# Performance work log

Hardware: AMD Instinct MI355X
Metric: run time of the kernel (lower is better)

Reference implementation:

```python
import jax, jax.numpy as jnp
import numpy as np

DIM, HEADS, DEPTH, SEQ, LOCAL_W = 1024, 16, 7, 2048, 64
HEAD_DIM = DIM // HEADS
SCALE = 1.0 / HEAD_DIM ** 0.5


def cantor_mask(S, depth, local_window):
    """Allowed (i,j): |i-j| within local window, OR |i-j| lies in the Cantor set
    under `depth` levels of ternary subdivision (no base-3 digit equals 1)."""
    idx = np.arange(S)
    d = np.abs(idx[:, None] - idx[None, :])
    x = d.copy()
    ok = np.ones_like(d, dtype=bool)
    for _ in range(depth):
        ok &= (x % 3) != 1
        x //= 3
    ok &= x == 0  # offset must be < 3**depth
    return jnp.asarray(ok | (d <= local_window))  # [S, S] bool


def setup_inputs() -> dict:
    key = jax.random.key(0)
    ks = jax.random.split(key, 8)
    B = 2
    s = 0.02
    return {
        "query": jax.random.normal(ks[0], (B, SEQ, DIM), jnp.float32),
        "key_value": jax.random.normal(ks[1], (B, SEQ, DIM), jnp.float32),
        "Wq": jax.random.normal(ks[2], (DIM, DIM), jnp.float32) * s,
        "bq": jnp.zeros((DIM,), jnp.float32),
        "Wkv": jax.random.normal(ks[3], (DIM, 2 * DIM), jnp.float32) * s,
        "bkv": jnp.zeros((2 * DIM,), jnp.float32),
        "Wo": jax.random.normal(ks[4], (DIM, DIM), jnp.float32) * s,
        "bo": jnp.zeros((DIM,), jnp.float32),
    }


def reference(query, key_value, Wq, bq, Wkv, bkv, Wo, bo):
    B, S, D = query.shape
    H, hd = HEADS, HEAD_DIM
    mask = cantor_mask(S, DEPTH, LOCAL_W)  # static [S, S] bool

    q = (query @ Wq + bq).reshape(B, S, H, hd).transpose(0, 2, 1, 3)  # [B,H,S,hd]
    kv = (key_value @ Wkv + bkv).reshape(B, S, 2, H, hd).transpose(2, 0, 3, 1, 4)
    k, v = kv[0], kv[1]  # [B,H,S,hd]

    scores = jnp.einsum("bhqd,bhkd->bhqk", q, k) * SCALE
    scores = jnp.where(mask, scores, jnp.finfo(scores.dtype).min)
    attn = jax.nn.softmax(scores, axis=-1)
    out = jnp.einsum("bhqk,bhkd->bhqd", attn, v)  # [B,H,S,hd]
    out = out.transpose(0, 2, 1, 3).reshape(B, S, D)
    return out @ Wo + bo
```

## Files before the change

### kernel.cpp

```cpp
#include <hip/hip_runtime.h>
#include <stdint.h>

typedef _Float16 half_t;
typedef __attribute__((ext_vector_type(8))) _Float16 half8;
typedef __attribute__((ext_vector_type(4))) _Float16 half4;
typedef __attribute__((ext_vector_type(4))) float floatx4;

#define SEQ 2048
#define NH 16
#define HD 64

#define MFMA16(a, b, c) __builtin_amdgcn_mfma_f32_16x16x16f16(a, b, c, 0, 0, 0)
#define MFMA32K(a, b, c) __builtin_amdgcn_mfma_f32_16x16x32_f16(a, b, c, 0, 0, 0)

#define QSCALE 0.1803368801111306f

__global__ __launch_bounds__(256) void prep(
    const float* __restrict__ query, const float* __restrict__ key_value,
    const float* __restrict__ Wq, const float* __restrict__ Wkv,
    const float* __restrict__ Wo, half_t* __restrict__ xq,
    half_t* __restrict__ xkv, half_t* __restrict__ wqT,
    half_t* __restrict__ wkvT, half_t* __restrict__ woT,
    uint8_t* __restrict__ tok, uint8_t* __restrict__ tok16,
    uint64_t* __restrict__ maskw) {
  int bx = blockIdx.x, tid = threadIdx.x;
  if (bx < 2048) {
    const float* s; half_t* d; int base;
    if (bx < 1024) { s = query; d = xq; base = bx * 4096; }
    else { s = key_value; d = xkv; base = (bx - 1024) * 4096; }
#pragma unroll
    for (int u = 0; u < 4; ++u) {
      int i = base + u * 1024 + tid * 4;
      floatx4 v = *(const floatx4*)(s + i);
      half4 h;
      h[0] = (half_t)v[0]; h[1] = (half_t)v[1];
      h[2] = (half_t)v[2]; h[3] = (half_t)v[3];
      *(half4*)(d + i) = h;
    }
    return;
  }
  if (bx < 4096) {
    __shared__ float tile[32][33];
    int tx = tid & 31, ty = tid >> 5;
    const int K = 1024;
#pragma unroll
    for (int u = 0; u < 2; ++u) {
      int t = (bx - 2048) * 2 + u;
      const float* W; half_t* Wt; int N, nt, kt;
      if (t < 1024) { W = Wq; Wt = wqT; N = 1024; nt = t & 31; kt = t >> 5; }
      else if (t < 3072) { int t2 = t - 1024; W = Wkv; Wt = wkvT; N = 2048; nt = t2 & 63; kt = t2 >> 6; }
      else { int t2 = t - 3072; W = Wo; Wt = woT; N = 1024; nt = t2 & 31; kt = t2 >> 5; }
      int n0 = nt * 32, k0 = kt * 32;
#pragma unroll
      for (int i = 0; i < 4; ++i)
        tile[ty + i * 8][tx] = W[(size_t)(k0 + ty + i * 8) * N + n0 + tx];
      __syncthreads();
#pragma unroll
      for (int i = 0; i < 4; ++i)
        Wt[(size_t)(n0 + ty + i * 8) * K + k0 + tx] = (half_t)tile[tx][ty + i * 8];
      __syncthreads();
    }
    return;
  }
  __shared__ uint8_t slut[2048];
  int ib = bx - 4096;
  for (int d = tid; d < 2048; d += 256) {
    int x = d;
    bool ok = true;
    for (int it = 0; it < 7; ++it) { ok &= ((x % 3) != 1); x /= 3; }
    ok &= (x == 0);
    slut[d] = (ok || d <= 64) ? 1 : 0;
  }
  __syncthreads();
  if (ib == 0) {
    if (tid < 64) {
      int delta = tid - 32;
      int lo = delta * 64 - 63, hi = delta * 64 + 63;
      uint8_t any = 0;
      for (int x = lo; x <= hi; ++x) {
        int a = x < 0 ? -x : x;
        if (a < 2048) any |= slut[a];
      }
      tok[tid] = any;
    }
    {
      int d16 = tid - 128;
      int ctr = d16 * 16;
      uint8_t any = 0;
      for (int x = ctr - 15; x <= ctr + 15; ++x) {
        int a = x < 0 ? -x : x;
        if (a < 2048) any |= slut[a];
      }
      tok16[tid] = any;
    }
  }
  int g = ib * 256 + tid;
  int tt = g - 2048;
  uint64_t w = 0;
  for (int jj = 0; jj < 64; ++jj) {
    int d = tt - jj; d = d < 0 ? -d : d;
    if (d < 2048 && slut[d]) w |= (1ull << jj);
  }
  maskw[g] = w;
}

__device__ __forceinline__ void cp16(half_t* lds, const half_t* g) {
  __builtin_amdgcn_global_load_lds(
      (const __attribute__((address_space(1))) uint32_t*)g,
      (__attribute__((address_space(3))) uint32_t*)lds, 16, 0, 0);
}

__global__ __launch_bounds__(256) void gemm_qkv(
    const half_t* __restrict__ xq, const half_t* __restrict__ xkv,
    const half_t* __restrict__ wqT, const half_t* __restrict__ wkvT,
    const float* __restrict__ bq, const float* __restrict__ bkv,
    half_t* __restrict__ qout, half_t* __restrict__ kout,
    half_t* __restrict__ vTout) {
  extern __shared__ char smemraw[];
  half_t* As = (half_t*)smemraw;
  half_t* Bs = As + 8192;
  const int K = 1024;
  bool isq = blockIdx.y < 8;
  const half_t* A = isq ? xq : xkv;
  const half_t* Bt = isq ? wqT : wkvT;
  const float* bias = isq ? bq : bkv;
  int n0 = (isq ? blockIdx.y : (blockIdx.y - 8)) * 128;
  int m0 = blockIdx.x * 128;

  int tid = threadIdx.x;
  int wave = tid >> 6, lane = tid & 63;
  int c = lane & 15, quad = lane >> 4;
  int wm = (wave >> 1) * 64, wn = (wave & 1) * 64;

  floatx4 acc[4][4] = {};
  int arow = tid >> 2;
  int akc = ((tid & 3) ^ (arow & 3)) * 8;
  int csw = c & 3;

  cp16(&As[wave * 512], A + (size_t)(m0 + arow) * K + akc);
  cp16(&As[2048 + wave * 512], A + (size_t)(m0 + 64 + arow) * K + akc);
  cp16(&Bs[wave * 512], Bt + (size_t)(n0 + arow) * K + akc);
  cp16(&Bs[2048 + wave * 512], Bt + (size_t)(n0 + 64 + arow) * K + akc);

  for (int kt = 0; kt < 32; ++kt) {
    __syncthreads();
    if (kt + 1 < 32) {
      int k0 = (kt + 1) * 32;
      int b = (kt + 1) & 1;
      cp16(&As[b * 4096 + wave * 512], A + (size_t)(m0 + arow) * K + k0 + akc);
      cp16(&As[b * 4096 + 2048 + wave * 512], A + (size_t)(m0 + 64 + arow) * K + k0 + akc);
      cp16(&Bs[b * 4096 + wave * 512], Bt + (size_t)(n0 + arow) * K + k0 + akc);
      cp16(&Bs[b * 4096 + 2048 + wave * 512], Bt + (size_t)(n0 + 64 + arow) * K + k0 + akc);
    }
    int b = kt & 1;
    half8 af[4], bf[4];
#pragma unroll
    for (int mt = 0; mt < 4; ++mt)
      af[mt] = *(const half8*)&As[b * 4096 + (wm + mt * 16 + c) * 32 + ((quad ^ csw) * 8)];
#pragma unroll
    for (int nt = 0; nt < 4; ++nt)
      bf[nt] = *(const half8*)&Bs[b * 4096 + (wn + nt * 16 + c) * 32 + ((quad ^ csw) * 8)];
#pragma unroll
    for (int mt = 0; mt < 4; ++mt)
#pragma unroll
      for (int nt = 0; nt < 4; ++nt)
        acc[mt][nt] = MFMA32K(af[mt], bf[nt], acc[mt][nt]);
  }

  __syncthreads();
  half_t* ep = (half_t*)smemraw;
  int bb = m0 >> 11, sbase = m0 & 2047;
  bool isv = (!isq) && (n0 >= 1024);

  if (!isv) {
#pragma unroll
    for (int nt = 0; nt < 4; ++nt) {
      int nl = wn + nt * 16 + c;
      float bv = bias[n0 + nl];
#pragma unroll
      for (int mt = 0; mt < 4; ++mt)
#pragma unroll
        for (int r = 0; r < 4; ++r) {
          int ml = wm + mt * 16 + quad * 4 + r;
          float v = acc[mt][nt][r] + bv;
          if (isq) v *= QSCALE;
          ep[ml * 128 + nl] = (half_t)v;
        }
    }
    __syncthreads();
    half_t* outp = isq ? qout : kout;
#pragma unroll
    for (int rd = 0; rd < 8; ++rd) {
      int id = rd * 256 + tid;
      int ml = id >> 4, ch = id & 15;
      int ng = n0 + ch * 8;
      int h = ng >> 6, d0 = ng & 63;
      half8 v = *(const half8*)&ep[ml * 128 + ch * 8];
      *(half8*)(outp + ((size_t)(bb * 16 + h) * SEQ + sbase + ml) * 64 + d0) = v;
    }
  } else {
#pragma unroll
    for (int nt = 0; nt < 4; ++nt) {
      int nl = wn + nt * 16 + c;
      float bv = bias[n0 + nl];
#pragma unroll
      for (int mt = 0; mt < 4; ++mt) {
        int ml = wm + mt * 16 + quad * 4;
        half4 hv;
#pragma unroll
        for (int r = 0; r < 4; ++r) hv[r] = (half_t)(acc[mt][nt][r] + bv);
        *(half4*)&ep[nl * 136 + ml] = hv;
      }
    }
    __syncthreads();
#pragma unroll
    for (int rd = 0; rd < 8; ++rd) {
      int id = rd * 256 + tid;
      int nl = id >> 4, mc = id & 15;
      int ng = n0 + nl;
      int h = (ng >> 6) & 15, d = ng & 63;
      half8 v = *(const half8*)&ep[nl * 136 + mc * 8];
      *(half8*)(vTout + ((size_t)(bb * 16 + h) * 64 + d) * SEQ + sbase + mc * 8) = v;
    }
  }
}

__global__ __launch_bounds__(256) void gemm_out(
    const half_t* __restrict__ A, const half_t* __restrict__ Bt,
    const float* __restrict__ bias, float* __restrict__ outf) {
  __shared__ half_t As[2][128 * 32];
  __shared__ half_t Bs[2][64 * 32];
  const int K = 1024;
  int tid = threadIdx.x;
  int wave = tid >> 6, lane = tid & 63;
  int c = lane & 15, quad = lane >> 4;
  int wm = (wave >> 1) * 64, wn = (wave & 1) * 32;
  int m0 = blockIdx.x * 128, n0 = blockIdx.y * 64;

  floatx4 acc[4][2] = {};
  int arow = tid >> 2;
  int akc = ((tid & 3) ^ (arow & 3)) * 8;
  int csw = c & 3;

  cp16(&As[0][wave * 512], A + (size_t)(m0 + arow) * K + akc);
  cp16(&As[0][2048 + wave * 512], A + (size_t)(m0 + 64 + arow) * K + akc);
  cp16(&Bs[0][wave * 512], Bt + (size_t)(n0 + arow) * K + akc);

  for (int kt = 0; kt < 32; ++kt) {
    __syncthreads();
    if (kt + 1 < 32) {
      int k0 = (kt + 1) * 32;
      int b = (kt + 1) & 1;
      cp16(&As[b][wave * 512], A + (size_t)(m0 + arow) * K + k0 + akc);
      cp16(&As[b][2048 + wave * 512], A + (size_t)(m0 + 64 + arow) * K + k0 + akc);
      cp16(&Bs[b][wave * 512], Bt + (size_t)(n0 + arow) * K + k0 + akc);
    }
    int b = kt & 1;
    half8 af[4], bf[2];
#pragma unroll
    for (int mt = 0; mt < 4; ++mt)
      af[mt] = *(const half8*)&As[b][(wm + mt * 16 + c) * 32 + ((quad ^ csw) * 8)];
#pragma unroll
    for (int nt = 0; nt < 2; ++nt)
      bf[nt] = *(const half8*)&Bs[b][(wn + nt * 16 + c) * 32 + ((quad ^ csw) * 8)];
#pragma unroll
    for (int mt = 0; mt < 4; ++mt)
#pragma unroll
      for (int nt = 0; nt < 2; ++nt)
        acc[mt][nt] = MFMA32K(af[mt], bf[nt], acc[mt][nt]);
  }

#pragma unroll
  for (int nt = 0; nt < 2; ++nt) {
    int n = n0 + wn + nt * 16 + c;
    float bv = bias[n];
#pragma unroll
    for (int mt = 0; mt < 4; ++mt)
#pragma unroll
      for (int r = 0; r < 4; ++r) {
        int m = m0 + wm + mt * 16 + quad * 4 + r;
        outf[(size_t)m * 1024 + n] = acc[mt][nt][r] + bv;
      }
  }
}

__global__ __launch_bounds__(512) void attn_kernel(
    const half_t* __restrict__ qb, const half_t* __restrict__ kb,
    const half_t* __restrict__ vTg, half_t* __restrict__ ctx,
    const uint64_t* __restrict__ maskw, const uint8_t* __restrict__ tok,
    const uint8_t* __restrict__ tok16g) {
  __shared__ half_t kT[64 * 64];
  __shared__ half_t vT[64 * 64];
  __shared__ half_t ot[128 * 72];
  __shared__ int list[34];
  __shared__ uint8_t tok16s[256];

  int tid = threadIdx.x, wave = tid >> 6, lane = tid & 63;
  int c = lane & 15, q = lane >> 4;
  int id = blockIdx.x;
  int bh = (id & 7) * 4 + ((id >> 3) & 3);
  int it128 = id >> 5;
  int i0 = it128 << 7;
  const half_t* qbase = qb + (size_t)bh * SEQ * HD;
  const half_t* kg = kb + (size_t)bh * SEQ * HD;
  const half_t* vg = vTg + (size_t)bh * HD * SEQ;

  if (tid < 256) tok16s[tid] = tok16g[tid];
  if (wave == 0) {
    int jt = lane;
    int base = i0 >> 6;
    bool act = (jt < 32) &&
               (tok[(jt - base) + 32] | tok[(jt - base - 1) + 32]);
    unsigned long long bal = __ballot(act);
    if (act) {
      int pre = __popcll(bal & ((1ull << jt) - 1));
      list[1 + pre] = jt << 6;
    }
    if (lane == 0) list[0] = __popcll(bal);
  }

  int i_row = i0 + wave * 16 + c;
  int it16 = (i0 >> 4) + wave;
  half8 qf0 = *(const half8*)(qbase + (size_t)i_row * 64 + q * 8);
  half8 qf1 = *(const half8*)(qbase + (size_t)i_row * 64 + 32 + q * 8);

  floatx4 oacc[4] = {};
  floatx4 lacc = {};
  half4 ones;
  ones[0] = (half_t)1.f; ones[1] = (half_t)1.f;
  ones[2] = (half_t)1.f; ones[3] = (half_t)1.f;

  int srow = tid >> 3;
  int sch = tid & 7;
  int ssw = srow & 7;

  __syncthreads();
  int nact = list[0];
  int j0 = list[1];

  half8 kr = *(const half8*)(kg + (size_t)(j0 + srow) * 64 + sch * 8);
  half8 vr = *(const half8*)(vg + (size_t)srow * SEQ + j0 + sch * 8);
  uint64_t wcur = maskw[(i_row - j0) + 2048];

  for (int ti = 0; ti < nact; ++ti) {
    int bidx = (j0 >> 4) - it16 + 128;
    __syncthreads();
    *(half8*)&kT[srow * 64 + ((sch ^ ssw) * 8)] = kr;
    *(half8*)&vT[srow * 64 + ((sch ^ ssw) * 8)] = vr;
    int j0n = (ti + 1 < nact) ? list[2 + ti] : j0;
    __syncthreads();

    uint64_t wnext = wcur;
    if (ti + 1 < nact) {
      kr = *(const half8*)(kg + (size_t)(j0n + srow) * 64 + sch * 8);
      vr = *(const half8*)(vg + (size_t)srow * SEQ + j0n + sch * 8);
      wnext = maskw[(i_row - j0n) + 2048];
    }

    uint32_t wlo = (uint32_t)(wcur >> (4 * q));
    uint32_t whi = (uint32_t)(wcur >> (32 + 4 * q));
#pragma unroll
    for (int jt = 0; jt < 4; ++jt) {
      if (!tok16s[bidx + jt]) continue;
      int row = jt * 16 + c;
      int sw = c & 7;
      half8 a0 = *(const half8*)&kT[row * 64 + ((q ^ sw) * 8)];
      half8 a1 = *(const half8*)&kT[row * 64 + (((4 + q) ^ sw) * 8)];
      floatx4 t = {};
      t = MFMA32K(a0, qf0, t);
      t = MFMA32K(a1, qf1, t);
      uint32_t ww = (jt < 2) ? wlo : whi;
#pragma unroll
      for (int r = 0; r < 4; ++r) {
        float p = __builtin_exp2f(t[r]);
        int bitpos = 16 * (jt & 1) + r;
        uint32_t msk = (uint32_t)(((int)(ww << (31 - bitpos))) >> 31);
        t[r] = __uint_as_float(__float_as_uint(p) & msk);
      }
      auto lo = __builtin_amdgcn_cvt_pkrtz(t[0], t[1]);
      auto hi = __builtin_amdgcn_cvt_pkrtz(t[2], t[3]);
      half4 pb;
      pb[0] = lo[0]; pb[1] = lo[1]; pb[2] = hi[0]; pb[3] = hi[1];
      lacc = MFMA16(ones, pb, lacc);
#pragma unroll
      for (int mt = 0; mt < 4; ++mt) {
        int drow = mt * 16 + c;
        int ch = 2 * jt + (q >> 1);
        half4 a = *(const half4*)&vT[drow * 64 + ((ch ^ sw) * 8) + (q & 1) * 4];
        oacc[mt] = MFMA16(a, pb, oacc[mt]);
      }
    }
    wcur = wnext;
    j0 = j0n;
  }

  float inv_l = 1.0f / lacc[0];
#pragma unroll
  for (int mt = 0; mt < 4; ++mt)
#pragma unroll
    for (int r = 0; r < 4; ++r)
      ot[(wave * 16 + c) * 72 + mt * 16 + 4 * q + r] = (half_t)(oacc[mt][r] * inv_l);
  __syncthreads();
  {
    int row = tid >> 2, chq = tid & 3;
    int b = bh >> 4, h = bh & 15;
    size_t base = (((size_t)(b * SEQ + i0 + row) * NH) + h) * 64 + chq * 16;
    half8 v0 = *(const half8*)&ot[row * 72 + chq * 16];
    half8 v1 = *(const half8*)&ot[row * 72 + chq * 16 + 8];
    *(half8*)(ctx + base) = v0;
    *(half8*)(ctx + base + 8) = v1;
  }
}

extern "C" void kernel_launch(void* const* d_in, const int* in_sizes, int n_in,
                              void* d_out, int out_size, void* d_ws, size_t ws_size,
                              hipStream_t stream) {
  const float* query = (const float*)d_in[0];
  const float* key_value = (const float*)d_in[1];
  const float* Wq = (const float*)d_in[2];
  const float* bq = (const float*)d_in[3];
  const float* Wkv = (const float*)d_in[4];
  const float* bkv = (const float*)d_in[5];
  const float* Wo = (const float*)d_in[6];
  const float* bo = (const float*)d_in[7];

  char* ws = (char*)d_ws;
  uint8_t* tok = (uint8_t*)ws;
  uint8_t* tok16 = (uint8_t*)(ws + 1024);
  uint64_t* maskw = (uint64_t*)(ws + 4096);
  const size_t MB = 1ull << 20;
  half_t* xq = (half_t*)(ws + 1 * MB);
  half_t* xkv = (half_t*)(ws + 9 * MB);
  half_t* wqT = (half_t*)(ws + 17 * MB);
  half_t* wkvT = (half_t*)(ws + 19 * MB);
  half_t* woT = (half_t*)(ws + 23 * MB);
  half_t* qbuf = (half_t*)(ws + 25 * MB);
  half_t* kbuf = (half_t*)(ws + 33 * MB);
  half_t* vTg = (half_t*)(ws + 41 * MB);
  half_t* ctx = xq;

  hipLaunchKernelGGL(prep, dim3(4112), dim3(256), 0, stream,
                     query, key_value, Wq, Wkv, Wo, xq, xkv, wqT, wkvT, woT,
                     tok, tok16, maskw);
  hipLaunchKernelGGL(gemm_qkv, dim3(32, 24), dim3(256), 34816, stream,
                     xq, xkv, wqT, wkvT, bq, bkv, qbuf, kbuf, vTg);
  hipLaunchKernelGGL(attn_kernel, dim3(512), dim3(512), 0, stream,
                     qbuf, kbuf, vTg, ctx, maskw, tok, tok16);
  hipLaunchKernelGGL(gemm_out, dim3(32, 16), dim3(256), 0, stream,
                     ctx, woT, bo, (float*)d_out);
}
```

Baseline: 215.5 us.

## Fuse QKV GEMM, attention and output GEMM into one persistent kernel with grid barriers

Replaces the three kernel launches after prep with one persistent kernel of 512 blocks of 512 threads. Blocks pull GEMM tiles from an atomic work counter and pass through software grid barriers between phases. The QKV GEMM tile grows to 128x256 and the output GEMM tile to 128x128. The aim is to remove launch gaps and tail effects between stages, at the cost of spin-wait barriers and a co-residency requirement that risks deadlock if all 512 blocks cannot be resident at once.

```diff
diff --git a/kernel.cpp b/kernel.cpp
--- a/kernel.cpp
+++ b/kernel.cpp
@@ -22,7 +22,7 @@
     half_t* __restrict__ xkv, half_t* __restrict__ wqT,
     half_t* __restrict__ wkvT, half_t* __restrict__ woT,
     uint8_t* __restrict__ tok, uint8_t* __restrict__ tok16,
-    uint64_t* __restrict__ maskw) {
+    uint64_t* __restrict__ maskw, uint32_t* __restrict__ ctrs) {
   int bx = blockIdx.x, tid = threadIdx.x;
   if (bx < 2048) {
     const float* s; half_t* d; int base;
@@ -64,6 +64,7 @@
   }
   __shared__ uint8_t slut[2048];
   int ib = bx - 4096;
+  if (ib == 0 && tid < 8) ctrs[tid] = 0;
   for (int d = tid; d < 2048; d += 256) {
     int x = d;
     bool ok = true;
@@ -110,305 +111,335 @@
       (__attribute__((address_space(3))) uint32_t*)lds, 16, 0, 0);
 }
 
-__global__ __launch_bounds__(256) void gemm_qkv(
+__device__ __forceinline__ void gridbar(uint32_t* ctr, uint32_t target) {
+  __threadfence();
+  __syncthreads();
+  if (threadIdx.x == 0) {
+    atomicAdd(ctr, 1u);
+    while (atomicAdd(ctr, 0u) < target) __builtin_amdgcn_s_sleep(16);
+  }
+  __syncthreads();
+  __threadfence();
+}
+
+__global__ __launch_bounds__(512, 4) void fused(
     const half_t* __restrict__ xq, const half_t* __restrict__ xkv,
     const half_t* __restrict__ wqT, const half_t* __restrict__ wkvT,
     const float* __restrict__ bq, const float* __restrict__ bkv,
     half_t* __restrict__ qout, half_t* __restrict__ kout,
-    half_t* __restrict__ vTout) {
+    half_t* __restrict__ vTout, const uint64_t* __restrict__ maskw,
+    const uint8_t* __restrict__ tok, const uint8_t* __restrict__ tok16g,
+    half_t* __restrict__ ctx, const half_t* __restrict__ woT,
+    const float* __restrict__ bo, float* __restrict__ outf,
+    uint32_t* ctrs) {
   extern __shared__ char smemraw[];
-  half_t* As = (half_t*)smemraw;
-  half_t* Bs = As + 8192;
-  const int K = 1024;
-  bool isq = blockIdx.y < 8;
-  const half_t* A = isq ? xq : xkv;
-  const half_t* Bt = isq ? wqT : wkvT;
-  const float* bias = isq ? bq : bkv;
-  int n0 = (isq ? blockIdx.y : (blockIdx.y - 8)) * 128;
-  int m0 = blockIdx.x * 128;
+  __shared__ int s_t;
+  __shared__ int list[34];
+  __shared__ uint8_t tok16s[256];
 
   int tid = threadIdx.x;
   int wave = tid >> 6, lane = tid & 63;
   int c = lane & 15, quad = lane >> 4;
-  int wm = (wave >> 1) * 64, wn = (wave & 1) * 64;
-
-  floatx4 acc[4][4] = {};
-  int arow = tid >> 2;
-  int akc = ((tid & 3) ^ (arow & 3)) * 8;
-  int csw = c & 3;
-
-  cp16(&As[wave * 512], A + (size_t)(m0 + arow) * K + akc);
-  cp16(&As[2048 + wave * 512], A + (size_t)(m0 + 64 + arow) * K + akc);
-  cp16(&Bs[wave * 512], Bt + (size_t)(n0 + arow) * K + akc);
-  cp16(&Bs[2048 + wave * 512], Bt + (size_t)(n0 + 64 + arow) * K + akc);
-
-  for (int kt = 0; kt < 32; ++kt) {
+  const int K = 1024;
+
+  {
+    half_t* As = (half_t*)smemraw;
+    half_t* Bs = As + 8192;
+    int wm = (wave >> 2) * 64, wn = (wave & 3) * 64;
+    int arow = tid >> 2;
+    int akc = ((tid & 3) ^ (arow & 3)) * 8;
+    int csw = c & 3;
+    for (;;) {
+      if (tid == 0) s_t = (int)atomicAdd(&ctrs[1], 1u);
+      __syncthreads();
+      int t = s_t;
+      __syncthreads();
+      if (t >= 384) break;
+      int xt = t & 31, y = t >> 5;
+      bool isq = y < 4;
+      const half_t* A = isq ? xq : xkv;
+      const half_t* Bt = isq ? wqT : wkvT;
+      const float* bias = isq ? bq : bkv;
+      int n0 = isq ? y * 256 : (y - 4) * 256;
+      int m0 = xt * 128;
+
+      floatx4 acc[4][4] = {};
+      cp16(&As[tid * 8], A + (size_t)(m0 + arow) * K + akc);
+      cp16(&Bs[tid * 8], Bt + (size_t)(n0 + arow) * K + akc);
+      cp16(&Bs[4096 + tid * 8], Bt + (size_t)(n0 + 128 + arow) * K + akc);
+
+      for (int kt = 0; kt < 32; ++kt) {
+        __syncthreads();
+        if (kt + 1 < 32) {
+          int k0 = (kt + 1) * 32;
+          int b = (kt + 1) & 1;
+          cp16(&As[b * 4096 + tid * 8], A + (size_t)(m0 + arow) * K + k0 + akc);
+          cp16(&Bs[b * 8192 + tid * 8], Bt + (size_t)(n0 + arow) * K + k0 + akc);
+          cp16(&Bs[b * 8192 + 4096 + tid * 8], Bt + (size_t)(n0 + 128 + arow) * K + k0 + akc);
+        }
+        int b = kt & 1;
+        half8 af[4], bf[4];
+#pragma unroll
+        for (int mt = 0; mt < 4; ++mt)
+          af[mt] = *(const half8*)&As[b * 4096 + (wm + mt * 16 + c) * 32 + ((quad ^ csw) * 8)];
+#pragma unroll
+        for (int nt = 0; nt < 4; ++nt)
+          bf[nt] = *(const half8*)&Bs[b * 8192 + (wn + nt * 16 + c) * 32 + ((quad ^ csw) * 8)];
+#pragma unroll
+        for (int mt = 0; mt < 4; ++mt)
+#pragma unroll
+          for (int nt = 0; nt < 4; ++nt)
+            acc[mt][nt] = MFMA32K(af[mt], bf[nt], acc[mt][nt]);
+      }
+
+      __syncthreads();
+      half_t* ep = (half_t*)smemraw;
+      int bb = m0 >> 11, sbase = m0 & 2047;
+      bool isv = (!isq) && (n0 >= 1024);
+#pragma unroll
+      for (int nh = 0; nh < 2; ++nh) {
+        if (!isv) {
+          if ((wn >> 7) == nh) {
+            int wnl = wn & 127;
+#pragma unroll
+            for (int nt = 0; nt < 4; ++nt) {
+              int nl = wnl + nt * 16 + c;
+              float bv = bias[n0 + wn + nt * 16 + c];
+#pragma unroll
+              for (int mt = 0; mt < 4; ++mt)
+#pragma unroll
+                for (int r = 0; r < 4; ++r) {
+                  int ml = wm + mt * 16 + quad * 4 + r;
+                  float v = acc[mt][nt][r] + bv;
+                  if (isq) v *= QSCALE;
+                  ep[ml * 128 + nl] = (half_t)v;
+                }
+            }
+          }
+          __syncthreads();
+          half_t* outp = isq ? qout : kout;
+#pragma unroll
+          for (int rd = 0; rd < 4; ++rd) {
+            int id = rd * 512 + tid;
+            int ml = id >> 4, ch = id & 15;
+            int ng = n0 + nh * 128 + ch * 8;
+            int h = ng >> 6, d0 = ng & 63;
+            half8 v = *(const half8*)&ep[ml * 128 + ch * 8];
+            *(half8*)(outp + ((size_t)(bb * 16 + h) * SEQ + sbase + ml) * 64 + d0) = v;
+          }
+          __syncthreads();
+        } else {
+          if ((wn >> 7) == nh) {
+            int wnl = wn & 127;
+#pragma unroll
+            for (int nt = 0; nt < 4; ++nt) {
+              int nl = wnl + nt * 16 + c;
+              float bv = bias[n0 + wn + nt * 16 + c];
+#pragma unroll
+              for (int mt = 0; mt < 4; ++mt) {
+                int ml = wm + mt * 16 + quad * 4;
+                half4 hv;
+#pragma unroll
+                for (int r = 0; r < 4; ++r) hv[r] = (half_t)(acc[mt][nt][r] + bv);
+                *(half4*)&ep[nl * 136 + ml] = hv;
+              }
+            }
+          }
+          __syncthreads();
+#pragma unroll
+          for (int rd = 0; rd < 4; ++rd) {
+            int id = rd * 512 + tid;
+            int nl = id >> 4, mc = id & 15;
+            int ng = n0 + nh * 128 + nl;
+            int h = (ng >> 6) & 15, d = ng & 63;
+            half8 v = *(const half8*)&ep[nl * 136 + mc * 8];
+            *(half8*)(vTout + ((size_t)(bb * 16 + h) * 64 + d) * SEQ + sbase + mc * 8) = v;
+          }
+          __syncthreads();
+        }
+      }
+    }
+  }
+
+  gridbar(&ctrs[0], 512);
+
+  {
+    half_t* kT = (half_t*)smemraw;
+    half_t* vT = kT + 4096;
+    half_t* ot = vT + 4096;
+    int id = blockIdx.x;
+    int bh = (id & 7) * 4 + ((id >> 3) & 3);
+    int it128 = id >> 5;
+    int i0 = it128 << 7;
+    const half_t* qbase = qout + (size_t)bh * SEQ * HD;
+    const half_t* kg = kout + (size_t)bh * SEQ * HD;
+    const half_t* vg = vTout + (size_t)bh * HD * SEQ;
+
+    if (tid < 256) tok16s[tid] = tok16g[tid];
+    if (wave == 0) {
+      int jt = lane;
+      int base = i0 >> 6;
+      bool act = (jt < 32) &&
+                 (tok[(jt - base) + 32] | tok[(jt - base - 1) + 32]);
+      unsigned long long bal = __ballot(act);
+      if (act) {
+        int pre = __popcll(bal & ((1ull << jt) - 1));
+        list[1 + pre] = jt << 6;
+      }
+      if (lane == 0) list[0] = __popcll(bal);
+    }
+
+    int i_row = i0 + wave * 16 + c;
+    int it16 = (i0 >> 4) + wave;
+    half8 qf0 = *(const half8*)(qbase + (size_t)i_row * 64 + quad * 8);
+    half8 qf1 = *(const half8*)(qbase + (size_t)i_row * 64 + 32 + quad * 8);
+
+    floatx4 oacc[4] = {};
+    floatx4 lacc = {};
+    half4 ones;
+    ones[0] = (half_t)1.f; ones[1] = (half_t)1.f;
+    ones[2] = (half_t)1.f; ones[3] = (half_t)1.f;
+
+    int srow = tid >> 3;
+    int sch = tid & 7;
+    int ssw = srow & 7;
+
     __syncthreads();
-    if (kt + 1 < 32) {
-      int k0 = (kt + 1) * 32;
-      int b = (kt + 1) & 1;
-      cp16(&As[b * 4096 + wave * 512], A + (size_t)(m0 + arow) * K + k0 + akc);
-      cp16(&As[b * 4096 + 2048 + wave * 512], A + (size_t)(m0 + 64 + arow) * K + k0 + akc);
-      cp16(&Bs[b * 4096 + wave * 512], Bt + (size_t)(n0 + arow) * K + k0 + akc);
-      cp16(&Bs[b * 4096 + 2048 + wave * 512], Bt + (size_t)(n0 + 64 + arow) * K + k0 + akc);
-    }
-    int b = kt & 1;
-    half8 af[4], bf[4];
+    int nact = list[0];
+    int j0 = list[1];
+
+    half8 kr = *(const half8*)(kg + (size_t)(j0 + srow) * 64 + sch * 8);
+    half8 vr = *(const half8*)(vg + (size_t)srow * SEQ + j0 + sch * 8);
+    uint64_t wcur = maskw[(i_row - j0) + 2048];
+
+    for (int ti = 0; ti < nact; ++ti) {
+      int bidx = (j0 >> 4) - it16 + 128;
+      __syncthreads();
+      *(half8*)&kT[srow * 64 + ((sch ^ ssw) * 8)] = kr;
+      *(half8*)&vT[srow * 64 + ((sch ^ ssw) * 8)] = vr;
+      int j0n = (ti + 1 < nact) ? list[2 + ti] : j0;
+      __syncthreads();
+
+      uint64_t wnext = wcur;
+      if (ti + 1 < nact) {
+        kr = *(const half8*)(kg + (size_t)(j0n + srow) * 64 + sch * 8);
+        vr = *(const half8*)(vg + (size_t)srow * SEQ + j0n + sch * 8);
+        wnext = maskw[(i_row - j0n) + 2048];
+      }
+
+      uint32_t wlo = (uint32_t)(wcur >> (4 * quad));
+      uint32_t whi = (uint32_t)(wcur >> (32 + 4 * quad));
+#pragma unroll
+      for (int jt = 0; jt < 4; ++jt) {
+        if (!tok16s[bidx + jt]) continue;
+        int row = jt * 16 + c;
+        int sw = c & 7;
+        half8 a0 = *(const half8*)&kT[row * 64 + ((quad ^ sw) * 8)];
+        half8 a1 = *(const half8*)&kT[row * 64 + (((4 + quad) ^ sw) * 8)];
+        floatx4 tt = {};
+        tt = MFMA32K(a0, qf0, tt);
+        tt = MFMA32K(a1, qf1, tt);
+        uint32_t ww = (jt < 2) ? wlo : whi;
+#pragma unroll
+        for (int r = 0; r < 4; ++r) {
+          float p = __builtin_exp2f(tt[r]);
+          int bitpos = 16 * (jt & 1) + r;
+          uint32_t msk = (uint32_t)(((int)(ww << (31 - bitpos))) >> 31);
+          tt[r] = __uint_as_float(__float_as_uint(p) & msk);
+        }
+        auto lo = __builtin_amdgcn_cvt_pkrtz(tt[0], tt[1]);
+        auto hi = __builtin_amdgcn_cvt_pkrtz(tt[2], tt[3]);
+        half4 pb;
+        pb[0] = lo[0]; pb[1] = lo[1]; pb[2] = hi[0]; pb[3] = hi[1];
+        lacc = MFMA16(ones, pb, lacc);
+#pragma unroll
+        for (int mt = 0; mt < 4; ++mt) {
+          int drow = mt * 16 + c;
+          int ch = 2 * jt + (quad >> 1);
+          half4 a = *(const half4*)&vT[drow * 64 + ((ch ^ sw) * 8) + (quad & 1) * 4];
+          oacc[mt] = MFMA16(a, pb, oacc[mt]);
+        }
+      }
+      wcur = wnext;
+      j0 = j0n;
+    }
+
+    float inv_l = 1.0f / lacc[0];
 #pragma unroll
     for (int mt = 0; mt < 4; ++mt)
-      af[mt] = *(const half8*)&As[b * 4096 + (wm + mt * 16 + c) * 32 + ((quad ^ csw) * 8)];
-#pragma unroll
-    for (int nt = 0; nt < 4; ++nt)
-      bf[nt] = *(const half8*)&Bs[b * 4096 + (wn + nt * 16 + c) * 32 + ((quad ^ csw) * 8)];
-#pragma unroll
-    for (int mt = 0; mt < 4; ++mt)
-#pragma unroll
-      for (int nt = 0; nt < 4; ++nt)
-        acc[mt][nt] = MFMA32K(af[mt], bf[nt], acc[mt][nt]);
-  }
-
-  __syncthreads();
-  half_t* ep = (half_t*)smemraw;
-  int bb = m0 >> 11, sbase = m0 & 2047;
-  bool isv = (!isq) && (n0 >= 1024);
-
-  if (!isv) {
-#pragma unroll
-    for (int nt = 0; nt < 4; ++nt) {
-      int nl = wn + nt * 16 + c;
-      float bv = bias[n0 + nl];
-#pragma unroll
-      for (int mt = 0; mt < 4; ++mt)
-#pragma unroll
-        for (int r = 0; r < 4; ++r) {
-          int ml = wm + mt * 16 + quad * 4 + r;
-          float v = acc[mt][nt][r] + bv;
-          if (isq) v *= QSCALE;
-          ep[ml * 128 + nl] = (half_t)v;
+#pragma unroll
+      for (int r = 0; r < 4; ++r)
+        ot[(wave * 16 + c) * 72 + mt * 16 + 4 * quad + r] = (half_t)(oacc[mt][r] * inv_l);
+    __syncthreads();
+    {
+      int row = tid >> 2, chq = tid & 3;
+      int b = bh >> 4, h = bh & 15;
+      size_t base = (((size_t)(b * SEQ + i0 + row) * NH) + h) * 64 + chq * 16;
+      half8 v0 = *(const half8*)&ot[row * 72 + chq * 16];
+      half8 v1 = *(const half8*)&ot[row * 72 + chq * 16 + 8];
+      *(half8*)(ctx + base) = v0;
+      *(half8*)(ctx + base + 8) = v1;
+    }
+  }
+
+  gridbar(&ctrs[0], 1024);
+
+  {
+    half_t* As = (half_t*)smemraw;
+    half_t* Bs = As + 8192;
+    int wm = (wave >> 2) * 64, wn = (wave & 3) * 32;
+    int arow = tid >> 2;
+    int akc = ((tid & 3) ^ (arow & 3)) * 8;
+    int csw = c & 3;
+    for (;;) {
+      if (tid == 0) s_t = (int)atomicAdd(&ctrs[2], 1u);
+      __syncthreads();
+      int t = s_t;
+      __syncthreads();
+      if (t >= 256) break;
+      int m0 = (t & 31) * 128, n0 = (t >> 5) * 128;
+
+      floatx4 acc[4][2] = {};
+      cp16(&As[tid * 8], ctx + (size_t)(m0 + arow) * K + akc);
+      cp16(&Bs[tid * 8], woT + (size_t)(n0 + arow) * K + akc);
+
+      for (int kt = 0; kt < 32; ++kt) {
+        __syncthreads();
+        if (kt + 1 < 32) {
+          int k0 = (kt + 1) * 32;
+          int b = (kt + 1) & 1;
+          cp16(&As[b * 4096 + tid * 8], ctx + (size_t)(m0 + arow) * K + k0 + akc);
+          cp16(&Bs[b * 4096 + tid * 8], woT + (size_t)(n0 + arow) * K + k0 + akc);
         }
-    }
-    __syncthreads();
-    half_t* outp = isq ? qout : kout;
-#pragma unroll
-    for (int rd = 0; rd < 8; ++rd) {
-      int id = rd * 256 + tid;
-      int ml = id >> 4, ch = id & 15;
-      int ng = n0 + ch * 8;
-      int h = ng >> 6, d0 = ng & 63;
-      half8 v = *(const half8*)&ep[ml * 128 + ch * 8];
-      *(half8*)(outp + ((size_t)(bb * 16 + h) * SEQ + sbase + ml) * 64 + d0) = v;
-    }
-  } else {
-#pragma unroll
-    for (int nt = 0; nt < 4; ++nt) {
-      int nl = wn + nt * 16 + c;
-      float bv = bias[n0 + nl];
-#pragma unroll
-      for (int mt = 0; mt < 4; ++mt) {
-        int ml = wm + mt * 16 + quad * 4;
-        half4 hv;
-#pragma unroll
-        for (int r = 0; r < 4; ++r) hv[r] = (half_t)(acc[mt][nt][r] + bv);
-        *(half4*)&ep[nl * 136 + ml] = hv;
-      }
-    }
-    __syncthreads();
-#pragma unroll
-    for (int rd = 0; rd < 8; ++rd) {
-      int id = rd * 256 + tid;
-      int nl = id >> 4, mc = id & 15;
-      int ng = n0 + nl;
-      int h = (ng >> 6) & 15, d = ng & 63;
-      half8 v = *(const half8*)&ep[nl * 136 + mc * 8];
-      *(half8*)(vTout + ((size_t)(bb * 16 + h) * 64 + d) * SEQ + sbase + mc * 8) = v;
-    }
-  }
-}
-
-__global__ __launch_bounds__(256) void gemm_out(
-    const half_t* __restrict__ A, const half_t* __restrict__ Bt,
-    const float* __restrict__ bias, float* __restrict__ outf) {
-  __shared__ half_t As[2][128 * 32];
-  __shared__ half_t Bs[2][64 * 32];
-  const int K = 1024;
-  int tid = threadIdx.x;
-  int wave = tid >> 6, lane = tid & 63;
-  int c = lane & 15, quad = lane >> 4;
-  int wm = (wave >> 1) * 64, wn = (wave & 1) * 32;
-  int m0 = blockIdx.x * 128, n0 = blockIdx.y * 64;
-
-  floatx4 acc[4][2] = {};
-  int arow = tid >> 2;
-  int akc = ((tid & 3) ^ (arow & 3)) * 8;
-  int csw = c & 3;
-
-  cp16(&As[0][wave * 512], A + (size_t)(m0 + arow) * K + akc);
-  cp16(&As[0][2048 + wave * 512], A + (size_t)(m0 + 64 + arow) * K + akc);
-  cp16(&Bs[0][wave * 512], Bt + (size_t)(n0 + arow) * K + akc);
-
-  for (int kt = 0; kt < 32; ++kt) {
-    __syncthreads();
-    if (kt + 1 < 32) {
-      int k0 = (kt + 1) * 32;
-      int b = (kt + 1) & 1;
-      cp16(&As[b][wave * 512], A + (size_t)(m0 + arow) * K + k0 + akc);
-      cp16(&As[b][2048 + wave * 512], A + (size_t)(m0 + 64 + arow) * K + k0 + akc);
-      cp16(&Bs[b][wave * 512], Bt + (size_t)(n0 + arow) * K + k0 + akc);
-    }
-    int b = kt & 1;
-    half8 af[4], bf[2];
-#pragma unroll
-    for (int mt = 0; mt < 4; ++mt)
-      af[mt] = *(const half8*)&As[b][(wm + mt * 16 + c) * 32 + ((quad ^ csw) * 8)];
-#pragma unroll
-    for (int nt = 0; nt < 2; ++nt)
-      bf[nt] = *(const half8*)&Bs[b][(wn + nt * 16 + c) * 32 + ((quad ^ csw) * 8)];
-#pragma unroll
-    for (int mt = 0; mt < 4; ++mt)
-#pragma unroll
-      for (int nt = 0; nt < 2; ++nt)
-        acc[mt][nt] = MFMA32K(af[mt], bf[nt], acc[mt][nt]);
-  }
-
-#pragma unroll
-  for (int nt = 0; nt < 2; ++nt) {
-    int n = n0 + wn + nt * 16 + c;
-    float bv = bias[n];
-#pragma unroll
-    for (int mt = 0; mt < 4; ++mt)
-#pragma unroll
-      for (int r = 0; r < 4; ++r) {
-        int m = m0 + wm + mt * 16 + quad * 4 + r;
-        outf[(size_t)m * 1024 + n] = acc[mt][nt][r] + bv;
-      }
-  }
-}
-
-__global__ __launch_bounds__(512) void attn_kernel(
-    const half_t* __restrict__ qb, const half_t* __restrict__ kb,
-    const half_t* __restrict__ vTg, half_t* __restrict__ ctx,
-    const uint64_t* __restrict__ maskw, const uint8_t* __restrict__ tok,
-    const uint8_t* __restrict__ tok16g) {
-  __shared__ half_t kT[64 * 64];
-  __shared__ half_t vT[64 * 64];
-  __shared__ half_t ot[128 * 72];
-  __shared__ int list[34];
-  __shared__ uint8_t tok16s[256];
-
-  int tid = threadIdx.x, wave = tid >> 6, lane = tid & 63;
-  int c = lane & 15, q = lane >> 4;
-  int id = blockIdx.x;
-  int bh = (id & 7) * 4 + ((id >> 3) & 3);
-  int it128 = id >> 5;
-  int i0 = it128 << 7;
-  const half_t* qbase = qb + (size_t)bh * SEQ * HD;
-  const half_t* kg = kb + (size_t)bh * SEQ * HD;
-  const half_t* vg = vTg + (size_t)bh * HD * SEQ;
-
-  if (tid < 256) tok16s[tid] = tok16g[tid];
-  if (wave == 0) {
-    int jt = lane;
-    int base = i0 >> 6;
-    bool act = (jt < 32) &&
-               (tok[(jt - base) + 32] | tok[(jt - base - 1) + 32]);
-    unsigned long long bal = __ballot(act);
-    if (act) {
-      int pre = __popcll(bal & ((1ull << jt) - 1));
-      list[1 + pre] = jt << 6;
-    }
-    if (lane == 0) list[0] = __popcll(bal);
-  }
-
-  int i_row = i0 + wave * 16 + c;
-  int it16 = (i0 >> 4) + wave;
-  half8 qf0 = *(const half8*)(qbase + (size_t)i_row * 64 + q * 8);
-  half8 qf1 = *(const half8*)(qbase + (size_t)i_row * 64 + 32 + q * 8);
-
-  floatx4 oacc[4] = {};
-  floatx4 lacc = {};
-  half4 ones;
-  ones[0] = (half_t)1.f; ones[1] = (half_t)1.f;
-  ones[2] = (half_t)1.f; ones[3] = (half_t)1.f;
-
-  int srow = tid >> 3;
-  int sch = tid & 7;
-  int ssw = srow & 7;
-
-  __syncthreads();
-  int nact = list[0];
-  int j0 = list[1];
-
-  half8 kr = *(const half8*)(kg + (size_t)(j0 + srow) * 64 + sch * 8);
-  half8 vr = *(const half8*)(vg + (size_t)srow * SEQ + j0 + sch * 8);
-  uint64_t wcur = maskw[(i_row - j0) + 2048];
-
-  for (int ti = 0; ti < nact; ++ti) {
-    int bidx = (j0 >> 4) - it16 + 128;
-    __syncthreads();
-    *(half8*)&kT[srow * 64 + ((sch ^ ssw) * 8)] = kr;
-    *(half8*)&vT[srow * 64 + ((sch ^ ssw) * 8)] = vr;
-    int j0n = (ti + 1 < nact) ? list[2 + ti] : j0;
-    __syncthreads();
-
-    uint64_t wnext = wcur;
-    if (ti + 1 < nact) {
-      kr = *(const half8*)(kg + (size_t)(j0n + srow) * 64 + sch * 8);
-      vr = *(const half8*)(vg + (size_t)srow * SEQ + j0n + sch * 8);
-      wnext = maskw[(i_row - j0n) + 2048];
-    }
-
-    uint32_t wlo = (uint32_t)(wcur >> (4 * q));
-    uint32_t whi = (uint32_t)(wcur >> (32 + 4 * q));
-#pragma unroll
-    for (int jt = 0; jt < 4; ++jt) {
-      if (!tok16s[bidx + jt]) continue;
-      int row = jt * 16 + c;
-      int sw = c & 7;
-      half8 a0 = *(const half8*)&kT[row * 64 + ((q ^ sw) * 8)];
-      half8 a1 = *(const half8*)&kT[row * 64 + (((4 + q) ^ sw) * 8)];
-      floatx4 t = {};
-      t = MFMA32K(a0, qf0, t);
-      t = MFMA32K(a1, qf1, t);
-      uint32_t ww = (jt < 2) ? wlo : whi;
-#pragma unroll
-      for (int r = 0; r < 4; ++r) {
-        float p = __builtin_exp2f(t[r]);
-        int bitpos = 16 * (jt & 1) + r;
-        uint32_t msk = (uint32_t)(((int)(ww << (31 - bitpos))) >> 31);
-        t[r] = __uint_as_float(__float_as_uint(p) & msk);
-      }
-      auto lo = __builtin_amdgcn_cvt_pkrtz(t[0], t[1]);
-      auto hi = __builtin_amdgcn_cvt_pkrtz(t[2], t[3]);
-      half4 pb;
-      pb[0] = lo[0]; pb[1] = lo[1]; pb[2] = hi[0]; pb[3] = hi[1];
-      lacc = MFMA16(ones, pb, lacc);
-#pragma unroll
-      for (int mt = 0; mt < 4; ++mt) {
-        int drow = mt * 16 + c;
-        int ch = 2 * jt + (q >> 1);
-        half4 a = *(const half4*)&vT[drow * 64 + ((ch ^ sw) * 8) + (q & 1) * 4];
-        oacc[mt] = MFMA16(a, pb, oacc[mt]);
-      }
-    }
-    wcur = wnext;
-    j0 = j0n;
-  }
-
-  float inv_l = 1.0f / lacc[0];
-#pragma unroll
-  for (int mt = 0; mt < 4; ++mt)
-#pragma unroll
-    for (int r = 0; r < 4; ++r)
-      ot[(wave * 16 + c) * 72 + mt * 16 + 4 * q + r] = (half_t)(oacc[mt][r] * inv_l);
-  __syncthreads();
-  {
-    int row = tid >> 2, chq = tid & 3;
-    int b = bh >> 4, h = bh & 15;
-    size_t base = (((size_t)(b * SEQ + i0 + row) * NH) + h) * 64 + chq * 16;
-    half8 v0 = *(const half8*)&ot[row * 72 + chq * 16];
-    half8 v1 = *(const half8*)&ot[row * 72 + chq * 16 + 8];
-    *(half8*)(ctx + base) = v0;
-    *(half8*)(ctx + base + 8) = v1;
+        int b = kt & 1;
+        half8 af[4], bf[2];
+#pragma unroll
+        for (int mt = 0; mt < 4; ++mt)
+          af[mt] = *(const half8*)&As[b * 4096 + (wm + mt * 16 + c) * 32 + ((quad ^ csw) * 8)];
+#pragma unroll
+        for (int nt = 0; nt < 2; ++nt)
+          bf[nt] = *(const half8*)&Bs[b * 4096 + (wn + nt * 16 + c) * 32 + ((quad ^ csw) * 8)];
+#pragma unroll
+        for (int mt = 0; mt < 4; ++mt)
+#pragma unroll
+          for (int nt = 0; nt < 2; ++nt)
+            acc[mt][nt] = MFMA32K(af[mt], bf[nt], acc[mt][nt]);
+      }
+      __syncthreads();
+
+#pragma unroll
+      for (int nt = 0; nt < 2; ++nt) {
+        int n = n0 + wn + nt * 16 + c;
+        float bv = bo[n];
+#pragma unroll
+        for (int mt = 0; mt < 4; ++mt)
+#pragma unroll
+          for (int r = 0; r < 4; ++r) {
+            int m = m0 + wm + mt * 16 + quad * 4 + r;
+            outf[(size_t)m * 1024 + n] = acc[mt][nt][r] + bv;
+          }
+      }
+    }
   }
 }
 
@@ -426,6 +457,7 @@
 
   char* ws = (char*)d_ws;
   uint8_t* tok = (uint8_t*)ws;
+  uint32_t* ctrs = (uint32_t*)(ws + 512);
   uint8_t* tok16 = (uint8_t*)(ws + 1024);
   uint64_t* maskw = (uint64_t*)(ws + 4096);
   const size_t MB = 1ull << 20;
@@ -441,11 +473,8 @@
 
   hipLaunchKernelGGL(prep, dim3(4112), dim3(256), 0, stream,
                      query, key_value, Wq, Wkv, Wo, xq, xkv, wqT, wkvT, woT,
-                     tok, tok16, maskw);
-  hipLaunchKernelGGL(gemm_qkv, dim3(32, 24), dim3(256), 34816, stream,
-                     xq, xkv, wqT, wkvT, bq, bkv, qbuf, kbuf, vTg);
-  hipLaunchKernelGGL(attn_kernel, dim3(512), dim3(512), 0, stream,
-                     qbuf, kbuf, vTg, ctx, maskw, tok, tok16);
-  hipLaunchKernelGGL(gemm_out, dim3(32, 16), dim3(256), 0, stream,
-                     ctx, woT, bo, (float*)d_out);
+                     tok, tok16, maskw, ctrs);
+  hipLaunchKernelGGL(fused, dim3(512), dim3(512), 49152, stream,
+                     xq, xkv, wqT, wkvT, bq, bkv, qbuf, kbuf, vTg,
+                     maskw, tok, tok16, ctx, woT, bo, (float*)d_out, ctrs);
 }
```

After: 840.5 us. 290% more time.
